# Performance work log

Measured on AMD Instinct MI355X. Metric: run time of the kernel, lower is better.

## Reference

```python
import jax, jax.numpy as jnp
import numpy as np

B = 1024      # batch of ego samples (one query each)
N = 32768     # flat pool of neighbor hidden states
H = 256       # hidden_dim == feat_dim
MAX_NEIGH = 64


def setup_inputs() -> dict:
    key = jax.random.key(0)
    ks = jax.random.split(key, 10)
    enc_hidden = jax.random.normal(ks[0], (B, H), dtype=jnp.float32)
    social_ht = jax.random.normal(ks[1], (N, H), dtype=jnp.float32)
    starts = jax.random.randint(ks[2], (B,), 0, N - MAX_NEIGH)
    lens = jax.random.randint(ks[3], (B,), 1, MAX_NEIGH)  # >=1 neighbor per sample
    ends = starts + lens
    w_scale = 1.0 / np.sqrt(H)
    Wq = jax.random.normal(ks[4], (H, H), dtype=jnp.float32) * w_scale
    Wk = jax.random.normal(ks[5], (H, H), dtype=jnp.float32) * w_scale
    Wv = jax.random.normal(ks[6], (H, H), dtype=jnp.float32) * w_scale
    bq = jax.random.normal(ks[7], (H,), dtype=jnp.float32) * w_scale
    bk = jax.random.normal(ks[8], (H,), dtype=jnp.float32) * w_scale
    bv = jax.random.normal(ks[9], (H,), dtype=jnp.float32) * w_scale
    return {
        "enc_hidden": enc_hidden, "social_ht": social_ht,
        "neighbors_idx_start": starts, "neighbors_idx_end": ends,
        "Wq": Wq, "bq": bq, "Wk": Wk, "bk": bk, "Wv": Wv, "bv": bv,
    }


def reference(enc_hidden, social_ht, neighbors_idx_start, neighbors_idx_end,
              Wq, bq, Wk, bk, Wv, bv):
    d = Wq.shape[1]
    inv_sqrt_d = 1.0 / jnp.sqrt(jnp.asarray(d, enc_hidden.dtype))
    # q_emb / k_emb / v_emb are Linear + ReLU; q is scaled AFTER the ReLU
    q = jax.nn.relu(enc_hidden @ Wq + bq) * inv_sqrt_d      # [B, H]
    k = jax.nn.relu(social_ht @ Wk + bk)                     # [N, H]
    v = jax.nn.relu(social_ht @ Wv + bv)                     # [N, H]
    scores = q @ k.T                                         # [B, N]
    pos = jnp.arange(social_ht.shape[0])                     # [N]
    # mask: sample i attends only to social_ht[start_i:end_i]
    mask = (pos[None, :] >= neighbors_idx_start[:, None]) & \
           (pos[None, :] < neighbors_idx_end[:, None])       # [B, N]
    attn = jax.nn.softmax(jnp.where(mask, scores, -jnp.inf), axis=-1)
    return attn @ v                                          # [B, H]
```

## Files before the change

kernel.cpp:

```cpp
#include <hip/hip_runtime.h>
#include <hip/hip_bf16.h>
#include <math.h>

#define H 256
#define BQ 1024
#define NPOOL 32768
#define MAXN 64

#define TRANS_BLOCKS 32
#define QPROJ_BLOCKS 256

typedef __attribute__((ext_vector_type(8))) short short8;
typedef __attribute__((ext_vector_type(8))) unsigned short ushort8v;
typedef __attribute__((ext_vector_type(4))) float f32x4;

__device__ __forceinline__ unsigned short f2bf(float f) {
  unsigned int u = __float_as_uint(f);
  unsigned int r = (u + 0x7fffu + ((u >> 16) & 1u)) >> 16;
  return (unsigned short)r;
}
__device__ __forceinline__ float b2f(unsigned short u) {
  return __uint_as_float((unsigned int)u << 16);
}
__device__ __forceinline__ unsigned int cvt_pk_bf16(float a, float b) {
  unsigned int r;
  asm("v_cvt_pk_bf16_f32 %0, %1, %2" : "=v"(r) : "v"(a), "v"(b));
  return r;
}
__device__ __forceinline__ void gload16(const void* g, void* l) {
  __builtin_amdgcn_global_load_lds(
      (const __attribute__((address_space(1))) unsigned int*)g,
      (__attribute__((address_space(3))) unsigned int*)l, 16, 0, 0);
}

__global__ __launch_bounds__(256) void prep_kernel(
    const float* __restrict__ Wk, const float* __restrict__ Wv,
    unsigned short* __restrict__ WkT, unsigned short* __restrict__ WvT,
    const float* __restrict__ enc, const float* __restrict__ Wq,
    const float* __restrict__ bq, float* __restrict__ qbuf) {
  __shared__ float smem[64 * 65];
  const int b = blockIdx.x;
  const int t = threadIdx.x;

  if (b < TRANS_BLOCKS) {
    const float* W = (b & 16) ? Wv : Wk;
    unsigned short* WT = (b & 16) ? WvT : WkT;
    const int tile = b & 15;
    const int k0 = (tile >> 2) * 64, c0 = (tile & 3) * 64;
    const int tx = t & 63, ty = t >> 6;
    float (*ls)[65] = (float(*)[65])smem;
#pragma unroll
    for (int kk = 0; kk < 16; ++kk)
      ls[tx][kk * 4 + ty] = W[(size_t)(k0 + kk * 4 + ty) * H + c0 + tx];
    __syncthreads();
#pragma unroll
    for (int cc = 0; cc < 16; ++cc) {
      const int c = cc * 4 + ty;
      WT[(size_t)(c0 + c) * H + k0 + tx] = f2bf(ls[c][tx]);
    }
  } else {
    const int bb = b - TRANS_BLOCKS;
    const int row0 = bb * 4;
    float (*xs)[H] = (float(*)[H])smem;
    {
      float4 v = *(const float4*)(enc + (size_t)(row0 + (t >> 6)) * H + (t & 63) * 4);
      *(float4*)(&xs[t >> 6][(t & 63) * 4]) = v;
    }
    __syncthreads();
    float acc[4] = {0.f, 0.f, 0.f, 0.f};
#pragma unroll 4
    for (int k = 0; k < H; ++k) {
      const float w = Wq[(size_t)k * H + t];
#pragma unroll
      for (int r = 0; r < 4; ++r) acc[r] = fmaf(xs[r][k], w, acc[r]);
    }
    const float bias = bq[t];
#pragma unroll
    for (int r = 0; r < 4; ++r)
      qbuf[(size_t)(row0 + r) * H + t] = fmaxf(acc[r] + bias, 0.f) * 0.0625f;
  }
}

__global__ __launch_bounds__(512) void kvproj_kernel(
    const float* __restrict__ soc,
    const unsigned short* __restrict__ WkT,
    const unsigned short* __restrict__ WvT,
    const float* __restrict__ bk, const float* __restrict__ bv,
    unsigned short* __restrict__ kout, unsigned short* __restrict__ vout) {
  __shared__ __align__(16) char LDSb[98304];
  const int t = threadIdx.x;
  const int lane = t & 63, wid = t >> 6;
  const int bid = blockIdx.x;
  const int bx = ((bid >> 4) << 3) | (bid & 7);
  const int by = (bid >> 3) & 1;
  const int brow = bx * 128;
  const int col0 = by * 128;

  const int srow = t >> 3;
  const int slin = t & 7;
  const int arow = t >> 2;
  const int sbase = (t & 3) * 2;

  f32x4 accK[2][4], accV[2][4];
#pragma unroll
  for (int n = 0; n < 2; ++n)
#pragma unroll
    for (int m = 0; m < 4; ++m) { accK[n][m] = (f32x4)0.f; accV[n][m] = (f32x4)0.f; }

  const int wr = wid >> 2, wc = wid & 3;

  float4 av[4];
  const float* asrc = soc + (size_t)(brow + arow) * H + sbase * 8;

#define AREG_LOAD(kt)                                                 \
  {                                                                   \
    const float* p_ = asrc + (kt)*64;                                 \
    _Pragma("unroll") for (int s = 0; s < 4; ++s)                     \
        av[s] = *(const float4*)(p_ + s * 4);                         \
  }
#define STAGE_B(kt, pb)                                               \
  {                                                                   \
    const int k0_ = (kt)*64;                                          \
    char* bk_ = LDSb + 32768 + (pb)*16384;                            \
    char* bv_ = LDSb + 65536 + (pb)*16384;                            \
    _Pragma("unroll") for (int c = 0; c < 2; ++c) {                   \
      const int row_ = c * 64 + srow;                                 \
      const int ssrc_ = slin ^ (row_ & 7);                            \
      gload16(WkT + (size_t)(col0 + row_) * H + k0_ + ssrc_ * 8,      \
              bk_ + c * 8192 + t * 16);                               \
      gload16(WvT + (size_t)(col0 + row_) * H + k0_ + ssrc_ * 8,      \
              bv_ + c * 8192 + t * 16);                               \
    }                                                                 \
  }
#define AWRITE(pb)                                                    \
  {                                                                   \
    char* ab_ = LDSb + (pb)*16384;                                    \
    _Pragma("unroll") for (int s = 0; s < 2; ++s) {                   \
      uint4 p;                                                        \
      p.x = cvt_pk_bf16(av[2 * s].x, av[2 * s].y);                    \
      p.y = cvt_pk_bf16(av[2 * s].z, av[2 * s].w);                    \
      p.z = cvt_pk_bf16(av[2 * s + 1].x, av[2 * s + 1].y);            \
      p.w = cvt_pk_bf16(av[2 * s + 1].z, av[2 * s + 1].w);            \
      *(uint4*)(ab_ + arow * 128 + ((sbase + s) ^ (arow & 7)) * 16) = p; \
    }                                                                 \
  }

  AREG_LOAD(0);
  STAGE_B(0, 0);
  asm volatile("s_waitcnt vmcnt(4)" ::: "memory");
  AWRITE(0);

#pragma unroll
  for (int kt = 0; kt < 4; ++kt) {
    const int cur = kt & 1;
    if (kt < 3) {
      AREG_LOAD(kt + 1);
      STAGE_B(kt + 1, cur ^ 1);
      asm volatile("s_waitcnt vmcnt(8)" ::: "memory");
    } else {
      asm volatile("s_waitcnt vmcnt(0)" ::: "memory");
    }
    asm volatile("s_waitcnt lgkmcnt(0)" ::: "memory");
    __builtin_amdgcn_s_barrier();
    const char* Ab = LDSb + cur * 16384;
    const char* Bkb = LDSb + 32768 + cur * 16384;
    const char* Bvb = LDSb + 65536 + cur * 16384;
#pragma unroll
    for (int kk = 0; kk < 2; ++kk) {
      short8 af[4], bkf[2], bvf[2];
#pragma unroll
      for (int m = 0; m < 4; ++m) {
        const int ar = wr * 64 + m * 16 + (lane & 15);
        const int sl = (kk * 4 + (lane >> 4)) ^ (ar & 7);
        af[m] = *(const short8*)(Ab + ar * 128 + sl * 16);
      }
#pragma unroll
      for (int n = 0; n < 2; ++n) {
        const int br = wc * 32 + n * 16 + (lane & 15);
        const int sl = (kk * 4 + (lane >> 4)) ^ (br & 7);
        bkf[n] = *(const short8*)(Bkb + br * 128 + sl * 16);
        bvf[n] = *(const short8*)(Bvb + br * 128 + sl * 16);
      }
#pragma unroll
      for (int n = 0; n < 2; ++n)
#pragma unroll
        for (int m = 0; m < 4; ++m) {
          accK[n][m] = __builtin_amdgcn_mfma_f32_16x16x32_bf16(
              af[m], bkf[n], accK[n][m], 0, 0, 0);
          accV[n][m] = __builtin_amdgcn_mfma_f32_16x16x32_bf16(
              af[m], bvf[n], accV[n][m], 0, 0, 0);
        }
    }
    if (kt < 3) {
      asm volatile("s_waitcnt vmcnt(4)" ::: "memory");
      AWRITE(cur ^ 1);
    }
    __builtin_amdgcn_s_barrier();
  }
#undef AREG_LOAD
#undef STAGE_B
#undef AWRITE

  float bkn[2], bvn[2];
#pragma unroll
  for (int n = 0; n < 2; ++n) {
    const int col = col0 + wc * 32 + n * 16 + (lane & 15);
    bkn[n] = bk[col]; bvn[n] = bv[col];
  }
#pragma unroll
  for (int n = 0; n < 2; ++n)
#pragma unroll
    for (int m = 0; m < 4; ++m) {
      const int col = col0 + wc * 32 + n * 16 + (lane & 15);
#pragma unroll
      for (int r = 0; r < 4; ++r) {
        const int row = brow + wr * 64 + m * 16 + (lane >> 4) * 4 + r;
        kout[(size_t)row * H + col] = f2bf(fmaxf(accK[n][m][r] + bkn[n], 0.f));
        vout[(size_t)row * H + col] = f2bf(fmaxf(accV[n][m][r] + bvn[n], 0.f));
      }
    }
}

__global__ __launch_bounds__(256) void attn_kernel(
    const float* __restrict__ qb, const unsigned short* __restrict__ kb,
    const unsigned short* __restrict__ vb, const int* __restrict__ starts,
    const int* __restrict__ ends, float* __restrict__ out) {
  __shared__ float sc[MAXN];
  const int row = blockIdx.x, t = threadIdx.x;
  const int lane = t & 63, wave = t >> 6;
  const int start = starts[row];
  const int len = ends[row] - start;

  const int qp = (lane & 31) * 8;
  const float4 qv0 = *(const float4*)(qb + (size_t)row * H + qp);
  const float4 qv1 = *(const float4*)(qb + (size_t)row * H + qp + 4);

  for (int jj = wave * 2; jj < len; jj += 8) {
    const int j0 = jj + (lane >> 5);
    if (j0 < len) {
      const ushort8v k8 =
          *(const ushort8v*)(kb + (size_t)(start + j0) * H + qp);
      float s = qv0.x * b2f(k8[0]) + qv0.y * b2f(k8[1]) +
                qv0.z * b2f(k8[2]) + qv0.w * b2f(k8[3]) +
                qv1.x * b2f(k8[4]) + qv1.y * b2f(k8[5]) +
                qv1.z * b2f(k8[6]) + qv1.w * b2f(k8[7]);
#pragma unroll
      for (int off = 16; off; off >>= 1) s += __shfl_xor(s, off, 64);
      if ((lane & 31) == 0) sc[j0] = s;
    }
  }
  __syncthreads();

  if (t < 64) {
    const float x = (t < len) ? sc[t] : -INFINITY;
    float m = x;
#pragma unroll
    for (int off = 32; off; off >>= 1) m = fmaxf(m, __shfl_xor(m, off, 64));
    const float p = (t < len) ? __expf(x - m) : 0.f;
    float ssum = p;
#pragma unroll
    for (int off = 32; off; off >>= 1) ssum += __shfl_xor(ssum, off, 64);
    sc[t] = p / ssum;
  }
  __syncthreads();

  const unsigned short* vp = vb + (size_t)start * H + t;
  float a0 = 0.f, a1 = 0.f, a2 = 0.f, a3 = 0.f;
  int j = 0;
  for (; j + 3 < len; j += 4) {
    a0 = fmaf(sc[j + 0], b2f(vp[(size_t)(j + 0) * H]), a0);
    a1 = fmaf(sc[j + 1], b2f(vp[(size_t)(j + 1) * H]), a1);
    a2 = fmaf(sc[j + 2], b2f(vp[(size_t)(j + 2) * H]), a2);
    a3 = fmaf(sc[j + 3], b2f(vp[(size_t)(j + 3) * H]), a3);
  }
  for (; j < len; ++j) a0 = fmaf(sc[j], b2f(vp[(size_t)j * H]), a0);
  out[(size_t)row * H + t] = (a0 + a1) + (a2 + a3);
}

extern "C" void kernel_launch(void* const* d_in, const int* in_sizes, int n_in,
                              void* d_out, int out_size, void* d_ws,
                              size_t ws_size, hipStream_t stream) {
  (void)in_sizes; (void)n_in; (void)out_size; (void)ws_size;
  const float* enc = (const float*)d_in[0];
  const float* soc = (const float*)d_in[1];
  const int* starts = (const int*)d_in[2];
  const int* ends = (const int*)d_in[3];
  const float* Wq = (const float*)d_in[4];
  const float* bq = (const float*)d_in[5];
  const float* Wk = (const float*)d_in[6];
  const float* bk = (const float*)d_in[7];
  const float* Wv = (const float*)d_in[8];
  const float* bv = (const float*)d_in[9];
  float* out = (float*)d_out;

  unsigned short* kb = (unsigned short*)d_ws;
  unsigned short* vb = kb + (size_t)NPOOL * H;
  unsigned short* WkT = vb + (size_t)NPOOL * H;
  unsigned short* WvT = WkT + H * H;
  float* qbuf = (float*)(WvT + H * H);

  prep_kernel<<<TRANS_BLOCKS + QPROJ_BLOCKS, 256, 0, stream>>>(
      Wk, Wv, WkT, WvT, enc, Wq, bq, qbuf);
  kvproj_kernel<<<512, 512, 0, stream>>>(
      soc, WkT, WvT, bk, bv, kb, vb);
  attn_kernel<<<BQ, 256, 0, stream>>>(qbuf, kb, vb, starts, ends, out);
}
```

Baseline: 56.95 us.

## Split K/V projection across blocks and fold Q projection into kvproj

The KV projection kernel now computes only K or only V per block, doubling the grid to 1024 blocks and cutting LDS from 96KB to 64KB so more blocks can be resident (launch bounds 512,4). The Q projection moves out of the prep kernel into the K-blocks of kvproj, which overlaps it with the projection pipeline and leaves prep doing only the weight transposes. The trade-off is that each block now loads and converts the social_ht A tile from fp32 to bf16 separately for K and V, doubling that read traffic, and the scalar Q matmul adds serial latency to half the blocks.

```diff
diff --git a/kernel.cpp b/kernel.cpp
--- a/kernel.cpp
+++ b/kernel.cpp
@@ -7,9 +7,6 @@
 #define NPOOL 32768
 #define MAXN 64
 
-#define TRANS_BLOCKS 32
-#define QPROJ_BLOCKS 256
-
 typedef __attribute__((ext_vector_type(8))) short short8;
 typedef __attribute__((ext_vector_type(8))) unsigned short ushort8v;
 typedef __attribute__((ext_vector_type(4))) float f32x4;
@@ -35,77 +32,56 @@
 
 __global__ __launch_bounds__(256) void prep_kernel(
     const float* __restrict__ Wk, const float* __restrict__ Wv,
-    unsigned short* __restrict__ WkT, unsigned short* __restrict__ WvT,
-    const float* __restrict__ enc, const float* __restrict__ Wq,
-    const float* __restrict__ bq, float* __restrict__ qbuf) {
-  __shared__ float smem[64 * 65];
+    unsigned short* __restrict__ WkT, unsigned short* __restrict__ WvT) {
+  __shared__ float ls[64][65];
   const int b = blockIdx.x;
   const int t = threadIdx.x;
-
-  if (b < TRANS_BLOCKS) {
-    const float* W = (b & 16) ? Wv : Wk;
-    unsigned short* WT = (b & 16) ? WvT : WkT;
-    const int tile = b & 15;
-    const int k0 = (tile >> 2) * 64, c0 = (tile & 3) * 64;
-    const int tx = t & 63, ty = t >> 6;
-    float (*ls)[65] = (float(*)[65])smem;
-#pragma unroll
-    for (int kk = 0; kk < 16; ++kk)
-      ls[tx][kk * 4 + ty] = W[(size_t)(k0 + kk * 4 + ty) * H + c0 + tx];
-    __syncthreads();
-#pragma unroll
-    for (int cc = 0; cc < 16; ++cc) {
-      const int c = cc * 4 + ty;
-      WT[(size_t)(c0 + c) * H + k0 + tx] = f2bf(ls[c][tx]);
-    }
-  } else {
-    const int bb = b - TRANS_BLOCKS;
-    const int row0 = bb * 4;
-    float (*xs)[H] = (float(*)[H])smem;
-    {
-      float4 v = *(const float4*)(enc + (size_t)(row0 + (t >> 6)) * H + (t & 63) * 4);
-      *(float4*)(&xs[t >> 6][(t & 63) * 4]) = v;
-    }
-    __syncthreads();
-    float acc[4] = {0.f, 0.f, 0.f, 0.f};
-#pragma unroll 4
-    for (int k = 0; k < H; ++k) {
-      const float w = Wq[(size_t)k * H + t];
-#pragma unroll
-      for (int r = 0; r < 4; ++r) acc[r] = fmaf(xs[r][k], w, acc[r]);
-    }
-    const float bias = bq[t];
-#pragma unroll
-    for (int r = 0; r < 4; ++r)
-      qbuf[(size_t)(row0 + r) * H + t] = fmaxf(acc[r] + bias, 0.f) * 0.0625f;
-  }
-}
-
-__global__ __launch_bounds__(512) void kvproj_kernel(
+  const float* W = (b & 16) ? Wv : Wk;
+  unsigned short* WT = (b & 16) ? WvT : WkT;
+  const int tile = b & 15;
+  const int k0 = (tile >> 2) * 64, c0 = (tile & 3) * 64;
+  const int tx = t & 63, ty = t >> 6;
+#pragma unroll
+  for (int kk = 0; kk < 16; ++kk)
+    ls[tx][kk * 4 + ty] = W[(size_t)(k0 + kk * 4 + ty) * H + c0 + tx];
+  __syncthreads();
+#pragma unroll
+  for (int cc = 0; cc < 16; ++cc) {
+    const int c = cc * 4 + ty;
+    WT[(size_t)(c0 + c) * H + k0 + tx] = f2bf(ls[c][tx]);
+  }
+}
+
+__global__ __launch_bounds__(512, 4) void kvproj_kernel(
     const float* __restrict__ soc,
     const unsigned short* __restrict__ WkT,
     const unsigned short* __restrict__ WvT,
     const float* __restrict__ bk, const float* __restrict__ bv,
+    const float* __restrict__ enc, const float* __restrict__ Wq,
+    const float* __restrict__ bq, float* __restrict__ qbuf,
     unsigned short* __restrict__ kout, unsigned short* __restrict__ vout) {
-  __shared__ __align__(16) char LDSb[98304];
+  __shared__ __align__(16) char LDSb[65536];
   const int t = threadIdx.x;
   const int lane = t & 63, wid = t >> 6;
   const int bid = blockIdx.x;
-  const int bx = ((bid >> 4) << 3) | (bid & 7);
-  const int by = (bid >> 3) & 1;
-  const int brow = bx * 128;
-  const int col0 = by * 128;
+  const int tile = ((bid >> 4) << 3) | (bid & 7);
+  const int kv = (bid >> 3) & 1;
+  const int brow = (tile >> 1) * 128;
+  const int col0 = (tile & 1) * 128;
+  const unsigned short* WT = kv ? WvT : WkT;
+  const float* bias = kv ? bv : bk;
+  unsigned short* outp = kv ? vout : kout;
 
   const int srow = t >> 3;
   const int slin = t & 7;
   const int arow = t >> 2;
   const int sbase = (t & 3) * 2;
 
-  f32x4 accK[2][4], accV[2][4];
+  f32x4 acc[2][4];
 #pragma unroll
   for (int n = 0; n < 2; ++n)
 #pragma unroll
-    for (int m = 0; m < 4; ++m) { accK[n][m] = (f32x4)0.f; accV[n][m] = (f32x4)0.f; }
+    for (int m = 0; m < 4; ++m) acc[n][m] = (f32x4)0.f;
 
   const int wr = wid >> 2, wc = wid & 3;
 
@@ -121,15 +97,12 @@
 #define STAGE_B(kt, pb)                                               \
   {                                                                   \
     const int k0_ = (kt)*64;                                          \
-    char* bk_ = LDSb + 32768 + (pb)*16384;                            \
-    char* bv_ = LDSb + 65536 + (pb)*16384;                            \
+    char* bb_ = LDSb + 32768 + (pb)*16384;                            \
     _Pragma("unroll") for (int c = 0; c < 2; ++c) {                   \
       const int row_ = c * 64 + srow;                                 \
       const int ssrc_ = slin ^ (row_ & 7);                            \
-      gload16(WkT + (size_t)(col0 + row_) * H + k0_ + ssrc_ * 8,      \
-              bk_ + c * 8192 + t * 16);                               \
-      gload16(WvT + (size_t)(col0 + row_) * H + k0_ + ssrc_ * 8,      \
-              bv_ + c * 8192 + t * 16);                               \
+      gload16(WT + (size_t)(col0 + row_) * H + k0_ + ssrc_ * 8,       \
+              bb_ + c * 8192 + t * 16);                               \
     }                                                                 \
   }
 #define AWRITE(pb)                                                    \
@@ -147,8 +120,25 @@
 
   AREG_LOAD(0);
   STAGE_B(0, 0);
-  asm volatile("s_waitcnt vmcnt(4)" ::: "memory");
+  asm volatile("s_waitcnt vmcnt(2)" ::: "memory");
   AWRITE(0);
+
+  if (kv == 0) {
+    const int qrow = 2 * tile + (t >> 8);
+    const int qcol = t & 255;
+    const float* er = enc + (size_t)qrow * H;
+    const float* wq = Wq + qcol;
+    float qa0 = 0.f, qa1 = 0.f, qa2 = 0.f, qa3 = 0.f;
+#pragma unroll 4
+    for (int k = 0; k < H; k += 4) {
+      qa0 = fmaf(er[k + 0], wq[(size_t)(k + 0) * H], qa0);
+      qa1 = fmaf(er[k + 1], wq[(size_t)(k + 1) * H], qa1);
+      qa2 = fmaf(er[k + 2], wq[(size_t)(k + 2) * H], qa2);
+      qa3 = fmaf(er[k + 3], wq[(size_t)(k + 3) * H], qa3);
+    }
+    const float qv = fmaxf((qa0 + qa1) + (qa2 + qa3) + bq[qcol], 0.f) * 0.0625f;
+    qbuf[(size_t)qrow * H + qcol] = qv;
+  }
 
 #pragma unroll
   for (int kt = 0; kt < 4; ++kt) {
@@ -156,18 +146,17 @@
     if (kt < 3) {
       AREG_LOAD(kt + 1);
       STAGE_B(kt + 1, cur ^ 1);
-      asm volatile("s_waitcnt vmcnt(8)" ::: "memory");
+      asm volatile("s_waitcnt vmcnt(6)" ::: "memory");
     } else {
       asm volatile("s_waitcnt vmcnt(0)" ::: "memory");
     }
     asm volatile("s_waitcnt lgkmcnt(0)" ::: "memory");
     __builtin_amdgcn_s_barrier();
     const char* Ab = LDSb + cur * 16384;
-    const char* Bkb = LDSb + 32768 + cur * 16384;
-    const char* Bvb = LDSb + 65536 + cur * 16384;
+    const char* Bb = LDSb + 32768 + cur * 16384;
 #pragma unroll
     for (int kk = 0; kk < 2; ++kk) {
-      short8 af[4], bkf[2], bvf[2];
+      short8 af[4], bf[2];
 #pragma unroll
       for (int m = 0; m < 4; ++m) {
         const int ar = wr * 64 + m * 16 + (lane & 15);
@@ -178,21 +167,17 @@
       for (int n = 0; n < 2; ++n) {
         const int br = wc * 32 + n * 16 + (lane & 15);
         const int sl = (kk * 4 + (lane >> 4)) ^ (br & 7);
-        bkf[n] = *(const short8*)(Bkb + br * 128 + sl * 16);
-        bvf[n] = *(const short8*)(Bvb + br * 128 + sl * 16);
+        bf[n] = *(const short8*)(Bb + br * 128 + sl * 16);
       }
 #pragma unroll
       for (int n = 0; n < 2; ++n)
 #pragma unroll
-        for (int m = 0; m < 4; ++m) {
-          accK[n][m] = __builtin_amdgcn_mfma_f32_16x16x32_bf16(
-              af[m], bkf[n], accK[n][m], 0, 0, 0);
-          accV[n][m] = __builtin_amdgcn_mfma_f32_16x16x32_bf16(
-              af[m], bvf[n], accV[n][m], 0, 0, 0);
-        }
+        for (int m = 0; m < 4; ++m)
+          acc[n][m] = __builtin_amdgcn_mfma_f32_16x16x32_bf16(
+              af[m], bf[n], acc[n][m], 0, 0, 0);
     }
     if (kt < 3) {
-      asm volatile("s_waitcnt vmcnt(4)" ::: "memory");
+      asm volatile("s_waitcnt vmcnt(2)" ::: "memory");
       AWRITE(cur ^ 1);
     }
     __builtin_amdgcn_s_barrier();
@@ -201,12 +186,10 @@
 #undef STAGE_B
 #undef AWRITE
 
-  float bkn[2], bvn[2];
-#pragma unroll
-  for (int n = 0; n < 2; ++n) {
-    const int col = col0 + wc * 32 + n * 16 + (lane & 15);
-    bkn[n] = bk[col]; bvn[n] = bv[col];
-  }
+  float bn[2];
+#pragma unroll
+  for (int n = 0; n < 2; ++n)
+    bn[n] = bias[col0 + wc * 32 + n * 16 + (lane & 15)];
 #pragma unroll
   for (int n = 0; n < 2; ++n)
 #pragma unroll
@@ -215,8 +198,7 @@
 #pragma unroll
       for (int r = 0; r < 4; ++r) {
         const int row = brow + wr * 64 + m * 16 + (lane >> 4) * 4 + r;
-        kout[(size_t)row * H + col] = f2bf(fmaxf(accK[n][m][r] + bkn[n], 0.f));
-        vout[(size_t)row * H + col] = f2bf(fmaxf(accV[n][m][r] + bvn[n], 0.f));
+        outp[(size_t)row * H + col] = f2bf(fmaxf(acc[n][m][r] + bn[n], 0.f));
       }
     }
 }
@@ -299,9 +281,8 @@
   unsigned short* WvT = WkT + H * H;
   float* qbuf = (float*)(WvT + H * H);
 
-  prep_kernel<<<TRANS_BLOCKS + QPROJ_BLOCKS, 256, 0, stream>>>(
-      Wk, Wv, WkT, WvT, enc, Wq, bq, qbuf);
-  kvproj_kernel<<<512, 512, 0, stream>>>(
-      soc, WkT, WvT, bk, bv, kb, vb);
+  prep_kernel<<<32, 256, 0, stream>>>(Wk, Wv, WkT, WvT);
+  kvproj_kernel<<<1024, 512, 0, stream>>>(
+      soc, WkT, WvT, bk, bv, enc, Wq, bq, qbuf, kb, vb);
   attn_kernel<<<BQ, 256, 0, stream>>>(qbuf, kb, vb, starts, ends, out);
 }
```

After: 70.69 us. 1.24x slower.

## Move Q projection into the MFMA GEMM kernel as extra bf16 tiles

Applied to the files above, without the earlier changes.

The scalar fp32 Q projection in the prep kernel is removed. Wq is instead transposed to bf16 with the 1/sqrt(d) scale folded into the weights and bias, and the Q rows are computed by 16 extra blocks of the MFMA GEMM kernel, which write bf16 q. This shortens the prep kernel to plain transposes and moves Q onto the matrix cores. In exchange, each Q block computes its tile twice (through both the K and V paths with the same weights), and q loses precision by being stored in bf16.

```diff
diff --git a/kernel.cpp b/kernel.cpp
--- a/kernel.cpp
+++ b/kernel.cpp
@@ -7,9 +7,6 @@
 #define NPOOL 32768
 #define MAXN 64
 
-#define TRANS_BLOCKS 32
-#define QPROJ_BLOCKS 256
-
 typedef __attribute__((ext_vector_type(8))) short short8;
 typedef __attribute__((ext_vector_type(8))) unsigned short ushort8v;
 typedef __attribute__((ext_vector_type(4))) float f32x4;
@@ -34,67 +31,63 @@
 }
 
 __global__ __launch_bounds__(256) void prep_kernel(
-    const float* __restrict__ Wk, const float* __restrict__ Wv,
-    unsigned short* __restrict__ WkT, unsigned short* __restrict__ WvT,
-    const float* __restrict__ enc, const float* __restrict__ Wq,
-    const float* __restrict__ bq, float* __restrict__ qbuf) {
-  __shared__ float smem[64 * 65];
+    const float* __restrict__ Wq, const float* __restrict__ Wk,
+    const float* __restrict__ Wv, const float* __restrict__ bq,
+    unsigned short* __restrict__ WqT, unsigned short* __restrict__ WkT,
+    unsigned short* __restrict__ WvT, float* __restrict__ bqs) {
+  __shared__ float ls[64][65];
   const int b = blockIdx.x;
   const int t = threadIdx.x;
-
-  if (b < TRANS_BLOCKS) {
-    const float* W = (b & 16) ? Wv : Wk;
-    unsigned short* WT = (b & 16) ? WvT : WkT;
-    const int tile = b & 15;
-    const int k0 = (tile >> 2) * 64, c0 = (tile & 3) * 64;
-    const int tx = t & 63, ty = t >> 6;
-    float (*ls)[65] = (float(*)[65])smem;
-#pragma unroll
-    for (int kk = 0; kk < 16; ++kk)
-      ls[tx][kk * 4 + ty] = W[(size_t)(k0 + kk * 4 + ty) * H + c0 + tx];
-    __syncthreads();
-#pragma unroll
-    for (int cc = 0; cc < 16; ++cc) {
-      const int c = cc * 4 + ty;
-      WT[(size_t)(c0 + c) * H + k0 + tx] = f2bf(ls[c][tx]);
-    }
-  } else {
-    const int bb = b - TRANS_BLOCKS;
-    const int row0 = bb * 4;
-    float (*xs)[H] = (float(*)[H])smem;
-    {
-      float4 v = *(const float4*)(enc + (size_t)(row0 + (t >> 6)) * H + (t & 63) * 4);
-      *(float4*)(&xs[t >> 6][(t & 63) * 4]) = v;
-    }
-    __syncthreads();
-    float acc[4] = {0.f, 0.f, 0.f, 0.f};
-#pragma unroll 4
-    for (int k = 0; k < H; ++k) {
-      const float w = Wq[(size_t)k * H + t];
-#pragma unroll
-      for (int r = 0; r < 4; ++r) acc[r] = fmaf(xs[r][k], w, acc[r]);
-    }
-    const float bias = bq[t];
-#pragma unroll
-    for (int r = 0; r < 4; ++r)
-      qbuf[(size_t)(row0 + r) * H + t] = fmaxf(acc[r] + bias, 0.f) * 0.0625f;
-  }
-}
-
-__global__ __launch_bounds__(512) void kvproj_kernel(
-    const float* __restrict__ soc,
+  const float* W = (b < 16) ? Wq : ((b < 32) ? Wk : Wv);
+  unsigned short* WT = (b < 16) ? WqT : ((b < 32) ? WkT : WvT);
+  const float scale = (b < 16) ? 0.0625f : 1.0f;
+  const int tile = b & 15;
+  const int k0 = (tile >> 2) * 64, c0 = (tile & 3) * 64;
+  const int tx = t & 63, ty = t >> 6;
+#pragma unroll
+  for (int kk = 0; kk < 16; ++kk)
+    ls[tx][kk * 4 + ty] = W[(size_t)(k0 + kk * 4 + ty) * H + c0 + tx];
+  __syncthreads();
+#pragma unroll
+  for (int cc = 0; cc < 16; ++cc) {
+    const int c = cc * 4 + ty;
+    WT[(size_t)(c0 + c) * H + k0 + tx] = f2bf(ls[c][tx] * scale);
+  }
+  if (b < 4 && t < 64) bqs[c0 + t] = bq[c0 + t] * 0.0625f;
+}
+
+__global__ __launch_bounds__(512) void gemm_kernel(
+    const float* __restrict__ soc, const float* __restrict__ enc,
     const unsigned short* __restrict__ WkT,
     const unsigned short* __restrict__ WvT,
+    const unsigned short* __restrict__ WqT,
     const float* __restrict__ bk, const float* __restrict__ bv,
-    unsigned short* __restrict__ kout, unsigned short* __restrict__ vout) {
+    const float* __restrict__ bqs,
+    unsigned short* __restrict__ kout, unsigned short* __restrict__ vout,
+    unsigned short* __restrict__ qout) {
   __shared__ __align__(16) char LDSb[98304];
   const int t = threadIdx.x;
   const int lane = t & 63, wid = t >> 6;
   const int bid = blockIdx.x;
-  const int bx = ((bid >> 4) << 3) | (bid & 7);
-  const int by = (bid >> 3) & 1;
-  const int brow = bx * 128;
-  const int col0 = by * 128;
+  const bool isQ = bid >= 512;
+  int brow, col0;
+  if (isQ) {
+    const int tl = bid - 512;
+    brow = (tl >> 1) * 128;
+    col0 = (tl & 1) * 128;
+  } else {
+    const int bx = ((bid >> 4) << 3) | (bid & 7);
+    const int by = (bid >> 3) & 1;
+    brow = bx * 128;
+    col0 = by * 128;
+  }
+  const float* Asrc = isQ ? enc : soc;
+  const unsigned short* Bkg = isQ ? WqT : WkT;
+  const unsigned short* Bvg = isQ ? WqT : WvT;
+  const float* biask = isQ ? bqs : bk;
+  const float* biasv = isQ ? bqs : bv;
+  unsigned short* outk = isQ ? qout : kout;
+  unsigned short* outv = isQ ? qout : vout;
 
   const int srow = t >> 3;
   const int slin = t & 7;
@@ -110,7 +103,7 @@
   const int wr = wid >> 2, wc = wid & 3;
 
   float4 av[4];
-  const float* asrc = soc + (size_t)(brow + arow) * H + sbase * 8;
+  const float* asrc = Asrc + (size_t)(brow + arow) * H + sbase * 8;
 
 #define AREG_LOAD(kt)                                                 \
   {                                                                   \
@@ -126,9 +119,9 @@
     _Pragma("unroll") for (int c = 0; c < 2; ++c) {                   \
       const int row_ = c * 64 + srow;                                 \
       const int ssrc_ = slin ^ (row_ & 7);                            \
-      gload16(WkT + (size_t)(col0 + row_) * H + k0_ + ssrc_ * 8,      \
+      gload16(Bkg + (size_t)(col0 + row_) * H + k0_ + ssrc_ * 8,      \
               bk_ + c * 8192 + t * 16);                               \
-      gload16(WvT + (size_t)(col0 + row_) * H + k0_ + ssrc_ * 8,      \
+      gload16(Bvg + (size_t)(col0 + row_) * H + k0_ + ssrc_ * 8,      \
               bv_ + c * 8192 + t * 16);                               \
     }                                                                 \
   }
@@ -205,7 +198,7 @@
 #pragma unroll
   for (int n = 0; n < 2; ++n) {
     const int col = col0 + wc * 32 + n * 16 + (lane & 15);
-    bkn[n] = bk[col]; bvn[n] = bv[col];
+    bkn[n] = biask[col]; bvn[n] = biasv[col];
   }
 #pragma unroll
   for (int n = 0; n < 2; ++n)
@@ -215,14 +208,15 @@
 #pragma unroll
       for (int r = 0; r < 4; ++r) {
         const int row = brow + wr * 64 + m * 16 + (lane >> 4) * 4 + r;
-        kout[(size_t)row * H + col] = f2bf(fmaxf(accK[n][m][r] + bkn[n], 0.f));
-        vout[(size_t)row * H + col] = f2bf(fmaxf(accV[n][m][r] + bvn[n], 0.f));
+        outk[(size_t)row * H + col] = f2bf(fmaxf(accK[n][m][r] + bkn[n], 0.f));
+        outv[(size_t)row * H + col] = f2bf(fmaxf(accV[n][m][r] + bvn[n], 0.f));
       }
     }
 }
 
 __global__ __launch_bounds__(256) void attn_kernel(
-    const float* __restrict__ qb, const unsigned short* __restrict__ kb,
+    const unsigned short* __restrict__ qb,
+    const unsigned short* __restrict__ kb,
     const unsigned short* __restrict__ vb, const int* __restrict__ starts,
     const int* __restrict__ ends, float* __restrict__ out) {
   __shared__ float sc[MAXN];
@@ -232,18 +226,20 @@
   const int len = ends[row] - start;
 
   const int qp = (lane & 31) * 8;
-  const float4 qv0 = *(const float4*)(qb + (size_t)row * H + qp);
-  const float4 qv1 = *(const float4*)(qb + (size_t)row * H + qp + 4);
+  const ushort8v q8 = *(const ushort8v*)(qb + (size_t)row * H + qp);
+  float qf[8];
+#pragma unroll
+  for (int e = 0; e < 8; ++e) qf[e] = b2f(q8[e]);
 
   for (int jj = wave * 2; jj < len; jj += 8) {
     const int j0 = jj + (lane >> 5);
     if (j0 < len) {
       const ushort8v k8 =
           *(const ushort8v*)(kb + (size_t)(start + j0) * H + qp);
-      float s = qv0.x * b2f(k8[0]) + qv0.y * b2f(k8[1]) +
-                qv0.z * b2f(k8[2]) + qv0.w * b2f(k8[3]) +
-                qv1.x * b2f(k8[4]) + qv1.y * b2f(k8[5]) +
-                qv1.z * b2f(k8[6]) + qv1.w * b2f(k8[7]);
+      float s = qf[0] * b2f(k8[0]) + qf[1] * b2f(k8[1]) +
+                qf[2] * b2f(k8[2]) + qf[3] * b2f(k8[3]) +
+                qf[4] * b2f(k8[4]) + qf[5] * b2f(k8[5]) +
+                qf[6] * b2f(k8[6]) + qf[7] * b2f(k8[7]);
 #pragma unroll
       for (int off = 16; off; off >>= 1) s += __shfl_xor(s, off, 64);
       if ((lane & 31) == 0) sc[j0] = s;
@@ -297,11 +293,12 @@
   unsigned short* vb = kb + (size_t)NPOOL * H;
   unsigned short* WkT = vb + (size_t)NPOOL * H;
   unsigned short* WvT = WkT + H * H;
-  float* qbuf = (float*)(WvT + H * H);
-
-  prep_kernel<<<TRANS_BLOCKS + QPROJ_BLOCKS, 256, 0, stream>>>(
-      Wk, Wv, WkT, WvT, enc, Wq, bq, qbuf);
-  kvproj_kernel<<<512, 512, 0, stream>>>(
-      soc, WkT, WvT, bk, bv, kb, vb);
-  attn_kernel<<<BQ, 256, 0, stream>>>(qbuf, kb, vb, starts, ends, out);
-}
+  unsigned short* WqT = WvT + H * H;
+  unsigned short* qbf = WqT + H * H;
+  float* bqs = (float*)(qbf + (size_t)BQ * H);
+
+  prep_kernel<<<48, 256, 0, stream>>>(Wq, Wk, Wv, bq, WqT, WkT, WvT, bqs);
+  gemm_kernel<<<528, 512, 0, stream>>>(soc, enc, WkT, WvT, WqT, bk, bv, bqs,
+                                       kb, vb, qbf);
+  attn_kernel<<<BQ, 256, 0, stream>>>(qbf, kb, vb, starts, ends, out);
+}
```

Result: faster. 49.00 us (median of 2 runs) (-13.9%).
